# Performance work log

Measured on AMD Instinct MI355X. Metric: run time of the kernel, lower is better.

## Reference

```python
import jax, jax.numpy as jnp
import numpy as np

D = 1152      # model dim
E = 4         # num_experts
HID = 768     # llama FFN hidden: multiple_of*ceil(int(2*1152/3)/256)
NH = 8        # cross-attention heads
TEMP = 2.0    # expert gumbel temperature (eval: no decay)


def _gumbel_softmax(key, logits, temp, hard):
    g = jax.random.gumbel(key, logits.shape, logits.dtype)
    y = jax.nn.softmax((logits + g) / temp, axis=-1)
    if hard:
        oh = jax.nn.one_hot(jnp.argmax(y, axis=-1), logits.shape[-1], dtype=logits.dtype)
        y = oh - jax.lax.stop_gradient(y) + y
    return y


def _mha(x, mem, in_w, in_b, out_w, out_b):
    # torch nn.MultiheadAttention(batch_first=True): packed qkv in_proj.
    B, S, Dm = x.shape
    hd = Dm // NH
    q = x @ in_w[:Dm].T + in_b[:Dm]
    k = mem @ in_w[Dm:2 * Dm].T + in_b[Dm:2 * Dm]
    v = mem @ in_w[2 * Dm:].T + in_b[2 * Dm:]
    q = q.reshape(B, S, NH, hd).transpose(0, 2, 1, 3)
    k = k.reshape(B, -1, NH, hd).transpose(0, 2, 1, 3)
    v = v.reshape(B, -1, NH, hd).transpose(0, 2, 1, 3)
    a = jax.nn.softmax(jnp.einsum('bhqd,bhkd->bhqk', q, k) / jnp.sqrt(jnp.asarray(hd, x.dtype)), axis=-1)
    o = jnp.einsum('bhqk,bhkd->bhqd', a, v).transpose(0, 2, 1, 3).reshape(B, S, Dm)
    return o @ out_w.T + out_b


def _ff_all(x2d, w1, w2, w3):
    # all E llama SwiGLU experts densely: x2d [N,D], w1/w3 [E,HID,D], w2 [E,D,HID] -> [N,E,D]
    h1 = jnp.einsum('nd,ehd->neh', x2d, w1)
    h3 = jnp.einsum('nd,ehd->neh', x2d, w3)
    return jnp.einsum('neh,edh->ned', jax.nn.silu(h1) * h3, w2)


def setup_inputs() -> dict:
    key = jax.random.key(0)
    ks = jax.random.split(key, 32)
    s = 0.02
    B, S, Sc = 2, 1024, 128
    inp = {
        'x': jax.random.normal(ks[0], (B, S, D), jnp.float32),
        'time': jax.random.normal(ks[1], (B, D), jnp.float32),
        'caption': jax.random.normal(ks[2], (B, Sc, D), jnp.float32),
        'acoustic': jax.random.normal(ks[3], (B, S, D), jnp.float32),
        'attn_in_w': jax.random.normal(ks[4], (3 * D, D), jnp.float32) * s,
        'attn_in_b': jnp.zeros((3 * D,), jnp.float32),
        'attn_out_w': jax.random.normal(ks[5], (D, D), jnp.float32) * s,
        'attn_out_b': jnp.zeros((D,), jnp.float32),
        'hl_w': jax.random.normal(ks[6], (2, D), jnp.float32) * s,
        'hl_b': jnp.zeros((2,), jnp.float32),
        'cap_gate_w': jax.random.normal(ks[7], (E, D), jnp.float32) * s,
        'cap_gate_b': jnp.zeros((E,), jnp.float32),
        'ac_gate_w': jax.random.normal(ks[8], (E, D), jnp.float32) * s,
        'ac_gate_b': jnp.zeros((E,), jnp.float32),
        'cap_w1': jax.random.normal(ks[9], (E, HID, D), jnp.float32) * s,
        'cap_w2': jax.random.normal(ks[10], (E, D, HID), jnp.float32) * s,
        'cap_w3': jax.random.normal(ks[11], (E, HID, D), jnp.float32) * s,
        'ac_w1': jax.random.normal(ks[12], (E, HID, D), jnp.float32) * s,
        'ac_w2': jax.random.normal(ks[13], (E, D, HID), jnp.float32) * s,
        'ac_w3': jax.random.normal(ks[14], (E, HID, D), jnp.float32) * s,
        'fr_w1': jax.random.normal(ks[15], (E, HID, D), jnp.float32) * s,
        'fr_w2': jax.random.normal(ks[16], (E, D, HID), jnp.float32) * s,
        'fr_w3': jax.random.normal(ks[17], (E, HID, D), jnp.float32) * s,
    }
    return inp


def reference(x, time, caption, acoustic,
              attn_in_w, attn_in_b, attn_out_w, attn_out_b,
              hl_w, hl_b, cap_gate_w, cap_gate_b, ac_gate_w, ac_gate_b,
              cap_w1, cap_w2, cap_w3, ac_w1, ac_w2, ac_w3,
              fr_w1, fr_w2, fr_w3):
    B, S, Dm = x.shape
    # cross-attention: x attends over caption, output replaces caption stream
    ca = _mha(x, caption, attn_in_w, attn_in_b, attn_out_w, attn_out_b)
    cap2 = ca.reshape(-1, Dm)          # [N, D]
    x2 = x.reshape(-1, Dm)             # [N, D]
    ac2 = acoustic.reshape(-1, Dm)     # [N, D]
    # high-level caption/acoustic gate from time embedding, broadcast over tokens
    hl = jnp.repeat(time @ hl_w.T + hl_b, S, axis=0)  # [N, 2]
    k1, k2, k3 = jax.random.split(jax.random.key(42), 3)
    hp = _gumbel_softmax(k1, hl, 1.0, False)
    cm = hp[:, 0:1]   # caption mask [N,1]
    am = hp[:, 1:2]   # acoustic mask [N,1]
    # expert gates (eval: hard one-hot straight-through)
    cp = _gumbel_softmax(k2, cap2 @ cap_gate_w.T + cap_gate_b, TEMP, True)  # [N,E]
    ap = _gumbel_softmax(k3, ac2 @ ac_gate_w.T + ac_gate_b, TEMP, True)    # [N,E]
    # dense per-expert SwiGLU, masked combine
    zc = jnp.einsum('ned,ne->nd', _ff_all(x2, cap_w1, cap_w2, cap_w3), cp) * cm
    za = jnp.einsum('ned,ne->nd', _ff_all(x2, ac_w1, ac_w2, ac_w3), ap) * am
    y = (zc + za).reshape(B, S, Dm)
    # frequency experts: each expert sees y masked to its channel block, keeps its block
    r = Dm // E
    region = ((jnp.arange(Dm)[None, :] // r) == jnp.arange(E)[:, None]).astype(x.dtype)  # [E,D]
    ym = y[None] * region[:, None, None, :]  # [E,B,S,D]
    h1 = jnp.einsum('ebsd,ehd->ebsh', ym, fr_w1)
    h3 = jnp.einsum('ebsd,ehd->ebsh', ym, fr_w3)
    fo = jnp.einsum('ebsh,edh->ebsd', jax.nn.silu(h1) * h3, fr_w2)  # [E,B,S,D]
    z = jnp.concatenate([fo[e, :, :, e * r:(e + 1) * r] for e in range(E)], axis=-1)
    # load balancing loss
    probs = jnp.concatenate([cp, ap], axis=1)                                  # [N,2E]
    masks = jnp.concatenate([jnp.tile(cm, (1, E)), jnp.tile(am, (1, E))], axis=1)
    usage = (probs * masks).sum(axis=0) / (masks.sum() + 1e-10)
    lb_loss = jnp.mean(usage * jnp.log(usage + 1e-10))
    return z, lb_loss
```

## Files before the change

kernel.cpp:

```cpp
#include <hip/hip_runtime.h>
#include <stdint.h>

#define NDIM 1152
#define NEXP 4
#define NHID 768
#define NHEAD 8
#define HDIM 144
#define NB 2
#define NS 1024
#define NSC 128
#define NTOK 2048
#define NCAP 256

typedef _Float16 f16;
typedef _Float16 f16x4 __attribute__((ext_vector_type(4)));
typedef _Float16 f16x8 __attribute__((ext_vector_type(8)));
typedef float f32x4 __attribute__((ext_vector_type(4)));

#define MFMA16(a, b, c) __builtin_amdgcn_mfma_f32_16x16x32_f16(a, b, c, 0, 0, 0)

#define WSZ ((size_t)NEXP * NHID * NDIM)

__device__ inline uint2 tfry(uint32_t k0, uint32_t k1, uint32_t x0, uint32_t x1) {
  uint32_t k2 = k0 ^ k1 ^ 0x1BD11BDAu;
#define RND(r) { x0 += x1; x1 = (x1 << r) | (x1 >> (32 - r)); x1 ^= x0; }
  x0 += k0; x1 += k1;
  RND(13) RND(15) RND(26) RND(6)
  x0 += k1; x1 += k2 + 1u;
  RND(17) RND(29) RND(16) RND(24)
  x0 += k2; x1 += k0 + 2u;
  RND(13) RND(15) RND(26) RND(6)
  x0 += k0; x1 += k1 + 3u;
  RND(17) RND(29) RND(16) RND(24)
  x0 += k1; x1 += k2 + 4u;
  RND(13) RND(15) RND(26) RND(6)
  x0 += k2; x1 += k0 + 5u;
#undef RND
  return make_uint2(x0, x1);
}

__device__ inline float b2g(uint32_t bits) {
  uint32_t fb = (bits >> 9) | 0x3f800000u;
  float f = __uint_as_float(fb) - 1.0f;
  const float tiny = 1.1754943508222875e-38f;
  float u = f * 1.0f + tiny;
  u = fmaxf(tiny, u);
  return -logf(-logf(u));
}

__global__ void k_prep(const float* __restrict__ timep, const float* __restrict__ hlw,
                       const float* __restrict__ hlb,
                       float* __restrict__ g1, float* __restrict__ g2, float* __restrict__ g3,
                       float* __restrict__ tl) {
  int t = threadIdx.x;
  uint2 k1 = tfry(0u, 42u, 0u, 0u);
  uint2 k2 = tfry(0u, 42u, 0u, 1u);
  uint2 k3 = tfry(0u, 42u, 0u, 2u);
  for (int p = t; p < 4096; p += 256) {
    uint2 o = tfry(k1.x, k1.y, 0u, (uint32_t)p);
    g1[p] = b2g(o.x ^ o.y);
  }
  for (int p = t; p < 8192; p += 256) {
    uint2 o2 = tfry(k2.x, k2.y, 0u, (uint32_t)p);
    g2[p] = b2g(o2.x ^ o2.y);
    uint2 o3 = tfry(k3.x, k3.y, 0u, (uint32_t)p);
    g3[p] = b2g(o3.x ^ o3.y);
  }
  int wv = t >> 6, lane = t & 63;
  {
    int b = wv >> 1, j = wv & 1;
    float s = 0.f;
    for (int k = lane; k < NDIM; k += 64) s += timep[b * NDIM + k] * hlw[j * NDIM + k];
    for (int m = 32; m; m >>= 1) s += __shfl_xor(s, m);
    if (lane == 0) tl[b * 2 + j] = s + hlb[j];
  }
}

__global__ void k_ac_logits(const float* __restrict__ ac, const float* __restrict__ agw,
                            const float* __restrict__ agb, float* __restrict__ al) {
  int wv = threadIdx.x >> 6, lane = threadIdx.x & 63;
  int n = blockIdx.x * 4 + wv;
  float s[NEXP] = {0.f, 0.f, 0.f, 0.f};
  for (int d = lane; d < NDIM; d += 64) {
    float a = ac[(size_t)n * NDIM + d];
#pragma unroll
    for (int e = 0; e < NEXP; ++e) s[e] += a * agw[e * NDIM + d];
  }
#pragma unroll
  for (int e = 0; e < NEXP; ++e)
    for (int m = 32; m; m >>= 1) s[e] += __shfl_xor(s[e], m);
  if (lane == 0) {
#pragma unroll
    for (int e = 0; e < NEXP; ++e) al[n * NEXP + e] = s[e] + agb[e];
  }
}

__global__ void k_cvt_w(const float* __restrict__ s0, const float* __restrict__ s1,
                        const float* __restrict__ s2, const float* __restrict__ s3,
                        const float* __restrict__ s4, const float* __restrict__ s5,
                        const float* __restrict__ s6, const float* __restrict__ s7,
                        const float* __restrict__ s8, f16* __restrict__ dst) {
  int slot = blockIdx.y;
  const float* src;
  switch (slot) {
    case 0: src = s0; break; case 1: src = s1; break; case 2: src = s2; break;
    case 3: src = s3; break; case 4: src = s4; break; case 5: src = s5; break;
    case 6: src = s6; break; case 7: src = s7; break; default: src = s8; break;
  }
  size_t i = ((size_t)blockIdx.x * 256 + threadIdx.x) * 4;
  if (i + 3 < WSZ) {
    float4 v = *(const float4*)(src + i);
    f16x4 h; h[0] = (f16)v.x; h[1] = (f16)v.y; h[2] = (f16)v.z; h[3] = (f16)v.w;
    *(f16x4*)(dst + slot * WSZ + i) = h;
  }
}

__global__ void k_cvt_add(const float* __restrict__ srca, const float* __restrict__ srcb,
                          f16* __restrict__ dst, int n) {
  int i = (blockIdx.x * 256 + threadIdx.x) * 4;
  if (i + 3 < n) {
    float4 va = *(const float4*)(srca + i);
    float4 vb = *(const float4*)(srcb + i);
    f16x4 h;
    h[0] = (f16)(va.x + vb.x); h[1] = (f16)(va.y + vb.y);
    h[2] = (f16)(va.z + vb.z); h[3] = (f16)(va.w + vb.w);
    *(f16x4*)(dst + i) = h;
  }
}

__global__ void k_cvt_split(const float* __restrict__ src, f16* __restrict__ hi,
                            f16* __restrict__ lo, int n) {
  int i = (blockIdx.x * 256 + threadIdx.x) * 4;
  if (i + 3 < n) {
    float4 v = *(const float4*)(src + i);
    f16x4 h, l;
    h[0] = (f16)v.x; l[0] = (f16)((v.x - (float)h[0]) * 2048.f);
    h[1] = (f16)v.y; l[1] = (f16)((v.y - (float)h[1]) * 2048.f);
    h[2] = (f16)v.z; l[2] = (f16)((v.z - (float)h[2]) * 2048.f);
    h[3] = (f16)v.w; l[3] = (f16)((v.w - (float)h[3]) * 2048.f);
    *(f16x4*)(hi + i) = h;
    *(f16x4*)(lo + i) = l;
  }
}

__global__ __launch_bounds__(256) void k_gemm_qkv(
    const f16* __restrict__ xhi, const f16* __restrict__ xlo,
    const f16* __restrict__ caphi, const f16* __restrict__ caplo,
    const float* __restrict__ inw, const float* __restrict__ inb,
    f16* __restrict__ qhi, f16* __restrict__ qlo,
    f16* __restrict__ khi, f16* __restrict__ klo,
    f16* __restrict__ vthi, f16* __restrict__ vtlo) {
  int z = blockIdx.z;
  int M = (z == 0) ? NTOK : NCAP;
  int mt = blockIdx.y, nt = blockIdx.x;
  if (mt * 64 >= M) return;
  const f16* Ah_g = (z == 0) ? xhi : caphi;
  const f16* Al_g = (z == 0) ? xlo : caplo;
  __shared__ f16 Ash[64 * 72];
  __shared__ f16 Asl[64 * 72];
  __shared__ f16 Bsh[64 * 72];
  __shared__ f16 Bsl[64 * 72];
  int t = threadIdx.x;
  int wv = t >> 6, lane = t & 63, m16 = lane & 15, quad = lane >> 4;
  int r0 = t >> 3, ak = (t & 7) * 8;
  size_t a0o = (size_t)(mt * 64 + r0) * NDIM;
  size_t a1o = (size_t)(mt * 64 + r0 + 32) * NDIM;
  f32x4 zf = {0.f, 0.f, 0.f, 0.f};
  f32x4 ah[2][2] = {{zf, zf}, {zf, zf}};
  f32x4 am[2][2] = {{zf, zf}, {zf, zf}};
  uint4 rah0, rah1, ral0, ral1;
  float4 rbw[4];
  rah0 = *(const uint4*)(Ah_g + a0o + ak);
  rah1 = *(const uint4*)(Ah_g + a1o + ak);
  ral0 = *(const uint4*)(Al_g + a0o + ak);
  ral1 = *(const uint4*)(Al_g + a1o + ak);
#pragma unroll
  for (int uu = 0; uu < 4; ++uu) {
    int u = t + uu * 256;
    int rr = u >> 4, kp = (u & 15) * 4;
    rbw[uu] = *(const float4*)(inw + (size_t)(z * NDIM + nt * 64 + rr) * NDIM + kp);
  }
  for (int kc = 0; kc < NDIM; kc += 64) {
    __syncthreads();
    *(uint4*)&Ash[r0 * 72 + ak] = rah0;
    *(uint4*)&Ash[(r0 + 32) * 72 + ak] = rah1;
    *(uint4*)&Asl[r0 * 72 + ak] = ral0;
    *(uint4*)&Asl[(r0 + 32) * 72 + ak] = ral1;
#pragma unroll
    for (int uu = 0; uu < 4; ++uu) {
      int u = t + uu * 256;
      int rr = u >> 4, kp = (u & 15) * 4;
      f16x4 hb, lb;
      hb[0] = (f16)rbw[uu].x; lb[0] = (f16)((rbw[uu].x - (float)hb[0]) * 2048.f);
      hb[1] = (f16)rbw[uu].y; lb[1] = (f16)((rbw[uu].y - (float)hb[1]) * 2048.f);
      hb[2] = (f16)rbw[uu].z; lb[2] = (f16)((rbw[uu].z - (float)hb[2]) * 2048.f);
      hb[3] = (f16)rbw[uu].w; lb[3] = (f16)((rbw[uu].w - (float)hb[3]) * 2048.f);
      *(f16x4*)&Bsh[rr * 72 + kp] = hb;
      *(f16x4*)&Bsl[rr * 72 + kp] = lb;
    }
    __syncthreads();
    int kn = kc + 64;
    if (kn < NDIM) {
      rah0 = *(const uint4*)(Ah_g + a0o + kn + ak);
      rah1 = *(const uint4*)(Ah_g + a1o + kn + ak);
      ral0 = *(const uint4*)(Al_g + a0o + kn + ak);
      ral1 = *(const uint4*)(Al_g + a1o + kn + ak);
#pragma unroll
      for (int uu = 0; uu < 4; ++uu) {
        int u = t + uu * 256;
        int rr = u >> 4, kp = (u & 15) * 4;
        rbw[uu] = *(const float4*)(inw + (size_t)(z * NDIM + nt * 64 + rr) * NDIM + kn + kp);
      }
    }
#pragma unroll
    for (int ks = 0; ks < 2; ++ks) {
      int aoff = ((wv & 1) * 32 + m16) * 72 + ks * 32 + quad * 8;
      int boff = ((wv >> 1) * 32 + m16) * 72 + ks * 32 + quad * 8;
      f16x8 a0h = *(const f16x8*)&Ash[aoff];
      f16x8 a1h = *(const f16x8*)&Ash[aoff + 16 * 72];
      f16x8 a0l = *(const f16x8*)&Asl[aoff];
      f16x8 a1l = *(const f16x8*)&Asl[aoff + 16 * 72];
      f16x8 b0h = *(const f16x8*)&Bsh[boff];
      f16x8 b1h = *(const f16x8*)&Bsh[boff + 16 * 72];
      f16x8 b0l = *(const f16x8*)&Bsl[boff];
      f16x8 b1l = *(const f16x8*)&Bsl[boff + 16 * 72];
      ah[0][0] = MFMA16(a0h, b0h, ah[0][0]);
      ah[0][1] = MFMA16(a0h, b1h, ah[0][1]);
      ah[1][0] = MFMA16(a1h, b0h, ah[1][0]);
      ah[1][1] = MFMA16(a1h, b1h, ah[1][1]);
      am[0][0] = MFMA16(a0h, b0l, am[0][0]);
      am[0][1] = MFMA16(a0h, b1l, am[0][1]);
      am[1][0] = MFMA16(a1h, b0l, am[1][0]);
      am[1][1] = MFMA16(a1h, b1l, am[1][1]);
      am[0][0] = MFMA16(a0l, b0h, am[0][0]);
      am[0][1] = MFMA16(a0l, b1h, am[0][1]);
      am[1][0] = MFMA16(a1l, b0h, am[1][0]);
      am[1][1] = MFMA16(a1l, b1h, am[1][1]);
    }
  }
#pragma unroll
  for (int mi = 0; mi < 2; ++mi)
#pragma unroll
    for (int ni = 0; ni < 2; ++ni)
#pragma unroll
      for (int r = 0; r < 4; ++r) {
        int row = mt * 64 + (wv & 1) * 32 + mi * 16 + quad * 4 + r;
        int col = nt * 64 + (wv >> 1) * 32 + ni * 16 + m16;
        float v = ah[mi][ni][r] + am[mi][ni][r] * (1.f / 2048.f) + inb[z * NDIM + col];
        size_t idx = (size_t)row * NDIM + col;
        if (z == 0) {
          f16 hq = (f16)v;
          qhi[idx] = hq;
          qlo[idx] = (f16)((v - (float)hq) * 2048.f);
        } else if (z == 1) {
          f16 hk = (f16)v;
          khi[idx] = hk;
          klo[idx] = (f16)((v - (float)hk) * 2048.f);
        } else {
          f16 hv = (f16)v;
          int bb = row >> 7, kv = row & 127;
          size_t ti = (size_t)(bb * NDIM + col) * NSC + kv;
          vthi[ti] = hv;
          vtlo[ti] = (f16)((v - (float)hv) * 2048.f);
        }
      }
}

__global__ __launch_bounds__(256) void k_attn(
    const f16* __restrict__ qhi, const f16* __restrict__ qlo,
    const f16* __restrict__ khi, const f16* __restrict__ klo,
    const f16* __restrict__ vthi, const f16* __restrict__ vtlo,
    f16* __restrict__ ohi, f16* __restrict__ olo) {
  int mt = blockIdx.x, bh = blockIdx.y;
  int b = bh >> 3, h = bh & 7;
  __shared__ f16 Ah[64 * 160];
  __shared__ f16 Al[64 * 160];
  __shared__ f16 Bh[32 * 160];
  __shared__ f16 Bl[32 * 160];
  __shared__ f16 Ph[64 * 136];
  __shared__ f16 Pl[64 * 136];
  int t = threadIdx.x;
  int wv = t >> 6, lane = t & 63, m16 = lane & 15, quad = lane >> 4;
  for (int u = t; u < 64 * 20; u += 256) {
    int r = u / 20, kp = (u % 20) * 8;
    uint4 vh = make_uint4(0u, 0u, 0u, 0u), vl = vh;
    if (kp < HDIM) {
      size_t gi = (size_t)(b * NS + mt * 64 + r) * NDIM + h * HDIM + kp;
      vh = *(const uint4*)&qhi[gi];
      vl = *(const uint4*)&qlo[gi];
    }
    *(uint4*)&Ah[r * 160 + kp] = vh;
    *(uint4*)&Al[r * 160 + kp] = vl;
  }
  __syncthreads();
  f16x8 ahf[5], alf[5];
#pragma unroll
  for (int ks = 0; ks < 5; ++ks) {
    int ao = (wv * 16 + m16) * 160 + ks * 32 + quad * 8;
    ahf[ks] = *(const f16x8*)&Ah[ao];
    alf[ks] = *(const f16x8*)&Al[ao];
  }
  f32x4 zf = {0.f, 0.f, 0.f, 0.f};
  f32x4 sh_[4][2], sm_[4][2];
#pragma unroll
  for (int kt = 0; kt < 4; ++kt)
#pragma unroll
    for (int ni = 0; ni < 2; ++ni) { sh_[kt][ni] = zf; sm_[kt][ni] = zf; }
  for (int kt = 0; kt < 4; ++kt) {
    if (kt) __syncthreads();
    for (int u = t; u < 32 * 20; u += 256) {
      int r = u / 20, kp = (u % 20) * 8;
      uint4 vh = make_uint4(0u, 0u, 0u, 0u), vl = vh;
      if (kp < HDIM) {
        size_t gi = (size_t)(b * NSC + kt * 32 + r) * NDIM + h * HDIM + kp;
        vh = *(const uint4*)&khi[gi];
        vl = *(const uint4*)&klo[gi];
      }
      *(uint4*)&Bh[r * 160 + kp] = vh;
      *(uint4*)&Bl[r * 160 + kp] = vl;
    }
    __syncthreads();
#pragma unroll
    for (int ks = 0; ks < 5; ++ks) {
#pragma unroll
      for (int ni = 0; ni < 2; ++ni) {
        int bo = (ni * 16 + m16) * 160 + ks * 32 + quad * 8;
        f16x8 bhf = *(const f16x8*)&Bh[bo];
        f16x8 blf = *(const f16x8*)&Bl[bo];
        sh_[kt][ni] = MFMA16(ahf[ks], bhf, sh_[kt][ni]);
        sm_[kt][ni] = MFMA16(ahf[ks], blf, sm_[kt][ni]);
        sm_[kt][ni] = MFMA16(alf[ks], bhf, sm_[kt][ni]);
      }
    }
  }
  float sv[4][2][4];
  float mx[4] = {-1e30f, -1e30f, -1e30f, -1e30f};
#pragma unroll
  for (int kt = 0; kt < 4; ++kt)
#pragma unroll
    for (int ni = 0; ni < 2; ++ni)
#pragma unroll
      for (int r = 0; r < 4; ++r) {
        float s = (sh_[kt][ni][r] + sm_[kt][ni][r] * (1.f / 2048.f)) * (1.f / 12.f);
        sv[kt][ni][r] = s;
        mx[r] = fmaxf(mx[r], s);
      }
#pragma unroll
  for (int r = 0; r < 4; ++r) {
    mx[r] = fmaxf(mx[r], __shfl_xor(mx[r], 1));
    mx[r] = fmaxf(mx[r], __shfl_xor(mx[r], 2));
    mx[r] = fmaxf(mx[r], __shfl_xor(mx[r], 4));
    mx[r] = fmaxf(mx[r], __shfl_xor(mx[r], 8));
  }
  float sum[4] = {0.f, 0.f, 0.f, 0.f};
#pragma unroll
  for (int kt = 0; kt < 4; ++kt)
#pragma unroll
    for (int ni = 0; ni < 2; ++ni)
#pragma unroll
      for (int r = 0; r < 4; ++r) {
        float e = expf(sv[kt][ni][r] - mx[r]);
        sv[kt][ni][r] = e;
        sum[r] += e;
      }
  float inv[4];
#pragma unroll
  for (int r = 0; r < 4; ++r) {
    sum[r] += __shfl_xor(sum[r], 1);
    sum[r] += __shfl_xor(sum[r], 2);
    sum[r] += __shfl_xor(sum[r], 4);
    sum[r] += __shfl_xor(sum[r], 8);
    inv[r] = 1.0f / sum[r];
  }
#pragma unroll
  for (int kt = 0; kt < 4; ++kt)
#pragma unroll
    for (int ni = 0; ni < 2; ++ni)
#pragma unroll
      for (int r = 0; r < 4; ++r) {
        float p = sv[kt][ni][r] * inv[r];
        int row = wv * 16 + quad * 4 + r;
        int col = kt * 32 + ni * 16 + m16;
        f16 ph = (f16)p;
        Ph[row * 136 + col] = ph;
        Pl[row * 136 + col] = (f16)((p - (float)ph) * 2048.f);
      }
  const f16* vbh = vthi + (size_t)(b * NDIM + h * HDIM) * NSC;
  const f16* vbl = vtlo + (size_t)(b * NDIM + h * HDIM) * NSC;
  f32x4 oh_[9], om_[9];
#pragma unroll
  for (int nb = 0; nb < 9; ++nb) { oh_[nb] = zf; om_[nb] = zf; }
#pragma unroll
  for (int ks = 0; ks < 4; ++ks) {
    int po = (wv * 16 + m16) * 136 + ks * 32 + quad * 8;
    f16x8 pah = *(const f16x8*)&Ph[po];
    f16x8 pal = *(const f16x8*)&Pl[po];
#pragma unroll
    for (int nb = 0; nb < 9; ++nb) {
      size_t vo = (size_t)(nb * 16 + m16) * NSC + ks * 32 + quad * 8;
      f16x8 bvh = *(const f16x8*)&vbh[vo];
      f16x8 bvl = *(const f16x8*)&vbl[vo];
      oh_[nb] = MFMA16(pah, bvh, oh_[nb]);
      om_[nb] = MFMA16(pah, bvl, om_[nb]);
      om_[nb] = MFMA16(pal, bvh, om_[nb]);
    }
  }
#pragma unroll
  for (int nb = 0; nb < 9; ++nb)
#pragma unroll
    for (int r = 0; r < 4; ++r) {
      int row = mt * 64 + wv * 16 + quad * 4 + r;
      int col = h * HDIM + nb * 16 + m16;
      float v = oh_[nb][r] + om_[nb][r] * (1.f / 2048.f);
      size_t idx = (size_t)(b * NS + row) * NDIM + col;
      f16 hv = (f16)v;
      ohi[idx] = hv;
      olo[idx] = (f16)((v - (float)hv) * 2048.f);
    }
}

__global__ __launch_bounds__(256) void k_ca(
    const f16* __restrict__ ohi, const f16* __restrict__ olo,
    const float* __restrict__ ow, const float* __restrict__ ob,
    float* __restrict__ ca) {
  int mt = blockIdx.y, nt = blockIdx.x;
  __shared__ f16 Ash[64 * 72];
  __shared__ f16 Asl[64 * 72];
  __shared__ f16 Bsh[64 * 72];
  __shared__ f16 Bsl[64 * 72];
  int t = threadIdx.x;
  int wv = t >> 6, lane = t & 63, m16 = lane & 15, quad = lane >> 4;
  int r0 = t >> 3, ak = (t & 7) * 8;
  size_t a0o = (size_t)(mt * 64 + r0) * NDIM;
  size_t a1o = (size_t)(mt * 64 + r0 + 32) * NDIM;
  f32x4 zf = {0.f, 0.f, 0.f, 0.f};
  f32x4 ah[2][2] = {{zf, zf}, {zf, zf}};
  f32x4 am[2][2] = {{zf, zf}, {zf, zf}};
  uint4 rah0, rah1, ral0, ral1;
  float4 rbw[4];
  rah0 = *(const uint4*)(ohi + a0o + ak);
  rah1 = *(const uint4*)(ohi + a1o + ak);
  ral0 = *(const uint4*)(olo + a0o + ak);
  ral1 = *(const uint4*)(olo + a1o + ak);
#pragma unroll
  for (int uu = 0; uu < 4; ++uu) {
    int u = t + uu * 256;
    int rr = u >> 4, kp = (u & 15) * 4;
    rbw[uu] = *(const float4*)(ow + (size_t)(nt * 64 + rr) * NDIM + kp);
  }
  for (int kc = 0; kc < NDIM; kc += 64) {
    __syncthreads();
    *(uint4*)&Ash[r0 * 72 + ak] = rah0;
    *(uint4*)&Ash[(r0 + 32) * 72 + ak] = rah1;
    *(uint4*)&Asl[r0 * 72 + ak] = ral0;
    *(uint4*)&Asl[(r0 + 32) * 72 + ak] = ral1;
#pragma unroll
    for (int uu = 0; uu < 4; ++uu) {
      int u = t + uu * 256;
      int rr = u >> 4, kp = (u & 15) * 4;
      f16x4 hb, lb;
      hb[0] = (f16)rbw[uu].x; lb[0] = (f16)((rbw[uu].x - (float)hb[0]) * 2048.f);
      hb[1] = (f16)rbw[uu].y; lb[1] = (f16)((rbw[uu].y - (float)hb[1]) * 2048.f);
      hb[2] = (f16)rbw[uu].z; lb[2] = (f16)((rbw[uu].z - (float)hb[2]) * 2048.f);
      hb[3] = (f16)rbw[uu].w; lb[3] = (f16)((rbw[uu].w - (float)hb[3]) * 2048.f);
      *(f16x4*)&Bsh[rr * 72 + kp] = hb;
      *(f16x4*)&Bsl[rr * 72 + kp] = lb;
    }
    __syncthreads();
    int kn = kc + 64;
    if (kn < NDIM) {
      rah0 = *(const uint4*)(ohi + a0o + kn + ak);
      rah1 = *(const uint4*)(ohi + a1o + kn + ak);
      ral0 = *(const uint4*)(olo + a0o + kn + ak);
      ral1 = *(const uint4*)(olo + a1o + kn + ak);
#pragma unroll
      for (int uu = 0; uu < 4; ++uu) {
        int u = t + uu * 256;
        int rr = u >> 4, kp = (u & 15) * 4;
        rbw[uu] = *(const float4*)(ow + (size_t)(nt * 64 + rr) * NDIM + kn + kp);
      }
    }
#pragma unroll
    for (int ks = 0; ks < 2; ++ks) {
      int aoff = ((wv & 1) * 32 + m16) * 72 + ks * 32 + quad * 8;
      int boff = ((wv >> 1) * 32 + m16) * 72 + ks * 32 + quad * 8;
      f16x8 a0h = *(const f16x8*)&Ash[aoff];
      f16x8 a1h = *(const f16x8*)&Ash[aoff + 16 * 72];
      f16x8 a0l = *(const f16x8*)&Asl[aoff];
      f16x8 a1l = *(const f16x8*)&Asl[aoff + 16 * 72];
      f16x8 b0h = *(const f16x8*)&Bsh[boff];
      f16x8 b1h = *(const f16x8*)&Bsh[boff + 16 * 72];
      f16x8 b0l = *(const f16x8*)&Bsl[boff];
      f16x8 b1l = *(const f16x8*)&Bsl[boff + 16 * 72];
      ah[0][0] = MFMA16(a0h, b0h, ah[0][0]);
      ah[0][1] = MFMA16(a0h, b1h, ah[0][1]);
      ah[1][0] = MFMA16(a1h, b0h, ah[1][0]);
      ah[1][1] = MFMA16(a1h, b1h, ah[1][1]);
      am[0][0] = MFMA16(a0h, b0l, am[0][0]);
      am[0][1] = MFMA16(a0h, b1l, am[0][1]);
      am[1][0] = MFMA16(a1h, b0l, am[1][0]);
      am[1][1] = MFMA16(a1h, b1l, am[1][1]);
      am[0][0] = MFMA16(a0l, b0h, am[0][0]);
      am[0][1] = MFMA16(a0l, b1h, am[0][1]);
      am[1][0] = MFMA16(a1l, b0h, am[1][0]);
      am[1][1] = MFMA16(a1l, b1h, am[1][1]);
    }
  }
#pragma unroll
  for (int mi = 0; mi < 2; ++mi)
#pragma unroll
    for (int ni = 0; ni < 2; ++ni)
#pragma unroll
      for (int r = 0; r < 4; ++r) {
        int row = mt * 64 + (wv & 1) * 32 + mi * 16 + quad * 4 + r;
        int col = nt * 64 + (wv >> 1) * 32 + ni * 16 + m16;
        ca[(size_t)row * NDIM + col] =
            ah[mi][ni][r] + am[mi][ni][r] * (1.f / 2048.f) + ob[col];
      }
}

__global__ __launch_bounds__(1024) void k_route(
    const float* __restrict__ cl, const float* __restrict__ al,
    const float* __restrict__ g1, const float* __restrict__ g2,
    const float* __restrict__ g3, const float* __restrict__ tl,
    float* __restrict__ cmv, float* __restrict__ amv,
    int* __restrict__ lists, int* __restrict__ counts, float* __restrict__ out_loss) {
  __shared__ int lcnt[8];
  __shared__ float bins[8];
  __shared__ float ssum[2];
  int t = threadIdx.x;
  if (t < 8) { lcnt[t] = 0; bins[t] = 0.f; }
  if (t < 2) ssum[t] = 0.f;
  __syncthreads();
  for (int n = t; n < NTOK; n += 1024) {
    float lc[NEXP];
#pragma unroll
    for (int e = 0; e < NEXP; ++e) lc[e] = cl[n * NEXP + e] + g2[n * 4 + e];
    int ec = 0; float bv = lc[0];
#pragma unroll
    for (int e = 1; e < NEXP; ++e) if (lc[e] > bv) { bv = lc[e]; ec = e; }
    float la[NEXP];
#pragma unroll
    for (int e = 0; e < NEXP; ++e) la[e] = al[n * NEXP + e] + g3[n * 4 + e];
    int ea = 0; float bva = la[0];
#pragma unroll
    for (int e = 1; e < NEXP; ++e) if (la[e] > bva) { bva = la[e]; ea = e; }
    int b = n >> 10;
    float a0 = tl[b * 2 + 0] + g1[n * 2 + 0];
    float a1 = tl[b * 2 + 1] + g1[n * 2 + 1];
    float mx = fmaxf(a0, a1);
    float e0 = expf(a0 - mx), e1 = expf(a1 - mx);
    float cm = e0 / (e0 + e1), am = e1 / (e0 + e1);
    cmv[n] = cm; amv[n] = am;
    int p0 = atomicAdd(&lcnt[ec], 1);
    lists[ec * NTOK + p0] = n;
    int p1 = atomicAdd(&lcnt[4 + ea], 1);
    lists[(4 + ea) * NTOK + p1] = n;
    atomicAdd(&bins[ec], cm);
    atomicAdd(&bins[4 + ea], am);
    atomicAdd(&ssum[0], cm);
    atomicAdd(&ssum[1], am);
  }
  __syncthreads();
  if (t < 8) counts[t] = lcnt[t];
  if (t == 0) {
    float denom = 4.f * (ssum[0] + ssum[1]) + 1e-10f;
    float acc = 0.f;
    for (int j = 0; j < 8; ++j) {
      float u = bins[j] / denom;
      acc += u * logf(u + 1e-10f);
    }
    out_loss[0] = acc / 8.f;
  }
}

__global__ __launch_bounds__(256) void k_gemm1(
    const f16* __restrict__ x16, const f16* __restrict__ y16,
    const f16* __restrict__ wf,
    const int* __restrict__ lists, const int* __restrict__ counts,
    f16* __restrict__ tbuf, int gbase, int G) {
  int bid = blockIdx.x;
  int xcd = bid & 7;
  int local = bid >> 3;
  int ppx = (G * 12) >> 3;
  int pair = xcd * ppx + (local >> 5);
  int mt = local & 31;
  int g = gbase + pair / 12;
  int nt = pair % 12;
  const f16* A; const f16* B1; const f16* B3; f16* tout;
  const int* list = nullptr;
  int cnt, koff, K;
  if (g < 8) {
    int e = g & 3;
    cnt = counts[g];
    list = lists + g * NTOK;
    A = x16; koff = 0; K = NDIM;
    B1 = wf + (size_t)((g < 4) ? 0 : 2) * WSZ + (size_t)e * NHID * NDIM;
    B3 = wf + (size_t)((g < 4) ? 1 : 3) * WSZ + (size_t)e * NHID * NDIM;
    tout = tbuf + (size_t)g * NTOK * NHID;
  } else {
    int e = g - 8;
    cnt = NTOK;
    A = y16; koff = e * 288; K = 288;
    B1 = wf + (size_t)4 * WSZ + (size_t)e * NHID * NDIM + koff;
    B3 = wf + (size_t)5 * WSZ + (size_t)e * NHID * NDIM + koff;
    tout = tbuf + (size_t)e * NTOK * NHID;
  }
  if (mt * 64 >= cnt) return;
  int t = threadIdx.x;
  int wv = t >> 6, lane = t & 63, m16 = lane & 15, quad = lane >> 4;
  int r0 = t >> 3, ak = (t & 7) * 8;
  int m0 = mt * 64 + r0, m1 = m0 + 32;
  int tok0, tok1;
  if (list) { tok0 = list[min(m0, cnt - 1)]; tok1 = list[min(m1, cnt - 1)]; }
  else { tok0 = m0; tok1 = m1; }
  const f16* ar0 = A + (size_t)tok0 * NDIM + koff;
  const f16* ar1 = A + (size_t)tok1 * NDIM + koff;
  const f16* b1r0 = B1 + (size_t)(nt * 64 + r0) * NDIM;
  const f16* b1r1 = B1 + (size_t)(nt * 64 + r0 + 32) * NDIM;
  const f16* b3r0 = B3 + (size_t)(nt * 64 + r0) * NDIM;
  const f16* b3r1 = B3 + (size_t)(nt * 64 + r0 + 32) * NDIM;
  __shared__ f16 As[64 * 72];
  __shared__ f16 Bs1[64 * 72];
  __shared__ f16 Bs2[64 * 72];
  f32x4 zf = {0.f, 0.f, 0.f, 0.f};
  f32x4 ac1[2][2] = {{zf, zf}, {zf, zf}};
  f32x4 ac2[2][2] = {{zf, zf}, {zf, zf}};
  uint4 z4u = make_uint4(0u, 0u, 0u, 0u);
  uint4 ra0, ra1, rb10, rb11, rb30, rb31;
  {
    bool v = (ak < K);
    ra0  = v ? *(const uint4*)(ar0 + ak) : z4u;
    ra1  = v ? *(const uint4*)(ar1 + ak) : z4u;
    rb10 = v ? *(const uint4*)(b1r0 + ak) : z4u;
    rb11 = v ? *(const uint4*)(b1r1 + ak) : z4u;
    rb30 = v ? *(const uint4*)(b3r0 + ak) : z4u;
    rb31 = v ? *(const uint4*)(b3r1 + ak) : z4u;
  }
  for (int kc = 0; kc < K; kc += 64) {
    __syncthreads();
    *(uint4*)&As[r0 * 72 + ak] = ra0;
    *(uint4*)&As[(r0 + 32) * 72 + ak] = ra1;
    *(uint4*)&Bs1[r0 * 72 + ak] = rb10;
    *(uint4*)&Bs1[(r0 + 32) * 72 + ak] = rb11;
    *(uint4*)&Bs2[r0 * 72 + ak] = rb30;
    *(uint4*)&Bs2[(r0 + 32) * 72 + ak] = rb31;
    __syncthreads();
    int kn = kc + 64;
    if (kn < K) {
      bool v = (kn + ak < K);
      ra0  = v ? *(const uint4*)(ar0 + kn + ak) : z4u;
      ra1  = v ? *(const uint4*)(ar1 + kn + ak) : z4u;
      rb10 = v ? *(const uint4*)(b1r0 + kn + ak) : z4u;
      rb11 = v ? *(const uint4*)(b1r1 + kn + ak) : z4u;
      rb30 = v ? *(const uint4*)(b3r0 + kn + ak) : z4u;
      rb31 = v ? *(const uint4*)(b3r1 + kn + ak) : z4u;
    }
#pragma unroll
    for (int ks = 0; ks < 2; ++ks) {
      int aoff = ((wv & 1) * 32 + m16) * 72 + ks * 32 + quad * 8;
      int boff = ((wv >> 1) * 32 + m16) * 72 + ks * 32 + quad * 8;
      f16x8 a0 = *(const f16x8*)&As[aoff];
      f16x8 a1 = *(const f16x8*)&As[aoff + 16 * 72];
      f16x8 b10 = *(const f16x8*)&Bs1[boff];
      f16x8 b11 = *(const f16x8*)&Bs1[boff + 16 * 72];
      f16x8 b30 = *(const f16x8*)&Bs2[boff];
      f16x8 b31 = *(const f16x8*)&Bs2[boff + 16 * 72];
      ac1[0][0] = MFMA16(a0, b10, ac1[0][0]);
      ac1[0][1] = MFMA16(a0, b11, ac1[0][1]);
      ac1[1][0] = MFMA16(a1, b10, ac1[1][0]);
      ac1[1][1] = MFMA16(a1, b11, ac1[1][1]);
      ac2[0][0] = MFMA16(a0, b30, ac2[0][0]);
      ac2[0][1] = MFMA16(a0, b31, ac2[0][1]);
      ac2[1][0] = MFMA16(a1, b30, ac2[1][0]);
      ac2[1][1] = MFMA16(a1, b31, ac2[1][1]);
    }
  }
#pragma unroll
  for (int mi = 0; mi < 2; ++mi)
#pragma unroll
    for (int ni = 0; ni < 2; ++ni)
#pragma unroll
      for (int r = 0; r < 4; ++r) {
        int row = mt * 64 + (wv & 1) * 32 + mi * 16 + quad * 4 + r;
        int col = nt * 64 + (wv >> 1) * 32 + ni * 16 + m16;
        float h1 = ac1[mi][ni][r];
        float h3 = ac2[mi][ni][r];
        float sl = h1 / (1.0f + expf(-h1));
        tout[(size_t)row * NHID + col] = (f16)(sl * h3);
      }
}

__global__ __launch_bounds__(256) void k_gemm2(
    const f16* __restrict__ tbuf, const f16* __restrict__ wf,
    const int* __restrict__ lists, const int* __restrict__ counts,
    const float* __restrict__ cmv, const float* __restrict__ amv,
    float* __restrict__ yc, float* __restrict__ ya) {
  int bid = blockIdx.x;
  int xcd = bid & 7;
  int local = bid >> 3;
  int pair = xcd * 18 + (local >> 5);
  int mt = local & 31;
  int g = pair / 18;
  int nt = pair % 18;
  int e = g & 3;
  int cnt = counts[g];
  if (mt * 64 >= cnt) return;
  const int* list = lists + g * NTOK;
  const f16* A = tbuf + (size_t)g * NTOK * NHID;
  const f16* Bw = wf + (size_t)((g < 4) ? 6 : 7) * WSZ + (size_t)e * NDIM * NHID;
  const float* sc = (g < 4) ? cmv : amv;
  float* y = (g < 4) ? yc : ya;
  int t = threadIdx.x;
  int wv = t >> 6, lane = t & 63, m16 = lane & 15, quad = lane >> 4;
  int r0 = t >> 3, ak = (t & 7) * 8;
  const f16* ar0 = A + (size_t)(mt * 64 + r0) * NHID;
  const f16* ar1 = A + (size_t)(mt * 64 + r0 + 32) * NHID;
  const f16* br0 = Bw + (size_t)(nt * 64 + r0) * NHID;
  const f16* br1 = Bw + (size_t)(nt * 64 + r0 + 32) * NHID;
  __shared__ f16 As[64 * 72];
  __shared__ f16 Bs[64 * 72];
  f32x4 zf = {0.f, 0.f, 0.f, 0.f};
  f32x4 acc[2][2] = {{zf, zf}, {zf, zf}};
  uint4 ra0, ra1, rb0, rb1;
  ra0 = *(const uint4*)(ar0 + ak);
  ra1 = *(const uint4*)(ar1 + ak);
  rb0 = *(const uint4*)(br0 + ak);
  rb1 = *(const uint4*)(br1 + ak);
  for (int kc = 0; kc < NHID; kc += 64) {
    __syncthreads();
    *(uint4*)&As[r0 * 72 + ak] = ra0;
    *(uint4*)&As[(r0 + 32) * 72 + ak] = ra1;
    *(uint4*)&Bs[r0 * 72 + ak] = rb0;
    *(uint4*)&Bs[(r0 + 32) * 72 + ak] = rb1;
    __syncthreads();
    int kn = kc + 64;
    if (kn < NHID) {
      ra0 = *(const uint4*)(ar0 + kn + ak);
      ra1 = *(const uint4*)(ar1 + kn + ak);
      rb0 = *(const uint4*)(br0 + kn + ak);
      rb1 = *(const uint4*)(br1 + kn + ak);
    }
#pragma unroll
    for (int ks = 0; ks < 2; ++ks) {
      int aoff = ((wv & 1) * 32 + m16) * 72 + ks * 32 + quad * 8;
      int boff = ((wv >> 1) * 32 + m16) * 72 + ks * 32 + quad * 8;
      f16x8 a0 = *(const f16x8*)&As[aoff];
      f16x8 a1 = *(const f16x8*)&As[aoff + 16 * 72];
      f16x8 b0 = *(const f16x8*)&Bs[boff];
      f16x8 b1 = *(const f16x8*)&Bs[boff + 16 * 72];
      acc[0][0] = MFMA16(a0, b0, acc[0][0]);
      acc[0][1] = MFMA16(a0, b1, acc[0][1]);
      acc[1][0] = MFMA16(a1, b0, acc[1][0]);
      acc[1][1] = MFMA16(a1, b1, acc[1][1]);
    }
  }
#pragma unroll
  for (int mi = 0; mi < 2; ++mi)
#pragma unroll
    for (int ni = 0; ni < 2; ++ni)
#pragma unroll
      for (int r = 0; r < 4; ++r) {
        int mg = mt * 64 + (wv & 1) * 32 + mi * 16 + quad * 4 + r;
        if (mg < cnt) {
          int tok = list[mg];
          int col = nt * 64 + (wv >> 1) * 32 + ni * 16 + m16;
          float v = acc[mi][ni][r] * sc[tok];
          y[(size_t)tok * NDIM + col] = v;
        }
      }
}

__global__ __launch_bounds__(256) void k_gemm2_fr(
    const f16* __restrict__ tbuf, const f16* __restrict__ wf, float* __restrict__ zz) {
  int e = blockIdx.z;
  int mt = blockIdx.y, nt = blockIdx.x;
  const f16* A = tbuf + (size_t)e * NTOK * NHID;
  const f16* Bw = wf + (size_t)8 * WSZ + (size_t)e * NDIM * NHID;
  int t = threadIdx.x;
  int wv = t >> 6, lane = t & 63, m16 = lane & 15, quad = lane >> 4;
  int r0 = t >> 3, ak = (t & 7) * 8;
  const f16* ar0 = A + (size_t)(mt * 64 + r0) * NHID;
  const f16* ar1 = A + (size_t)(mt * 64 + r0 + 32) * NHID;
  int ne0 = min(nt * 64 + r0, 287), ne1 = min(nt * 64 + r0 + 32, 287);
  const f16* br0 = Bw + (size_t)(e * 288 + ne0) * NHID;
  const f16* br1 = Bw + (size_t)(e * 288 + ne1) * NHID;
  __shared__ f16 As[64 * 72];
  __shared__ f16 Bs[64 * 72];
  f32x4 zf = {0.f, 0.f, 0.f, 0.f};
  f32x4 acc[2][2] = {{zf, zf}, {zf, zf}};
  uint4 ra0, ra1, rb0, rb1;
  ra0 = *(const uint4*)(ar0 + ak);
  ra1 = *(const uint4*)(ar1 + ak);
  rb0 = *(const uint4*)(br0 + ak);
  rb1 = *(const uint4*)(br1 + ak);
  for (int kc = 0; kc < NHID; kc += 64) {
    __syncthreads();
    *(uint4*)&As[r0 * 72 + ak] = ra0;
    *(uint4*)&As[(r0 + 32) * 72 + ak] = ra1;
    *(uint4*)&Bs[r0 * 72 + ak] = rb0;
    *(uint4*)&Bs[(r0 + 32) * 72 + ak] = rb1;
    __syncthreads();
    int kn = kc + 64;
    if (kn < NHID) {
      ra0 = *(const uint4*)(ar0 + kn + ak);
      ra1 = *(const uint4*)(ar1 + kn + ak);
      rb0 = *(const uint4*)(br0 + kn + ak);
      rb1 = *(const uint4*)(br1 + kn + ak);
    }
#pragma unroll
    for (int ks = 0; ks < 2; ++ks) {
      int aoff = ((wv & 1) * 32 + m16) * 72 + ks * 32 + quad * 8;
      int boff = ((wv >> 1) * 32 + m16) * 72 + ks * 32 + quad * 8;
      f16x8 a0 = *(const f16x8*)&As[aoff];
      f16x8 a1 = *(const f16x8*)&As[aoff + 16 * 72];
      f16x8 b0 = *(const f16x8*)&Bs[boff];
      f16x8 b1 = *(const f16x8*)&Bs[boff + 16 * 72];
      acc[0][0] = MFMA16(a0, b0, acc[0][0]);
      acc[0][1] = MFMA16(a0, b1, acc[0][1]);
      acc[1][0] = MFMA16(a1, b0, acc[1][0]);
      acc[1][1] = MFMA16(a1, b1, acc[1][1]);
    }
  }
#pragma unroll
  for (int mi = 0; mi < 2; ++mi)
#pragma unroll
    for (int ni = 0; ni < 2; ++ni)
#pragma unroll
      for (int r = 0; r < 4; ++r) {
        int cg = nt * 64 + (wv >> 1) * 32 + ni * 16 + m16;
        if (cg < 288) {
          int row = mt * 64 + (wv & 1) * 32 + mi * 16 + quad * 4 + r;
          zz[(size_t)row * NDIM + e * 288 + cg] = acc[mi][ni][r];
        }
      }
}

extern "C" void kernel_launch(void* const* d_in, const int* in_sizes, int n_in,
                              void* d_out, int out_size, void* d_ws, size_t ws_size,
                              hipStream_t stream) {
  const float* x          = (const float*)d_in[0];
  const float* timep      = (const float*)d_in[1];
  const float* caption    = (const float*)d_in[2];
  const float* acoustic   = (const float*)d_in[3];
  const float* attn_in_w  = (const float*)d_in[4];
  const float* attn_in_b  = (const float*)d_in[5];
  const float* attn_out_w = (const float*)d_in[6];
  const float* attn_out_b = (const float*)d_in[7];
  const float* hl_w       = (const float*)d_in[8];
  const float* hl_b       = (const float*)d_in[9];
  const float* cap_gate_w = (const float*)d_in[10];
  const float* cap_gate_b = (const float*)d_in[11];
  const float* ac_gate_w  = (const float*)d_in[12];
  const float* ac_gate_b  = (const float*)d_in[13];
  const float* cap_w1     = (const float*)d_in[14];
  const float* cap_w2     = (const float*)d_in[15];
  const float* cap_w3     = (const float*)d_in[16];
  const float* ac_w1      = (const float*)d_in[17];
  const float* ac_w2      = (const float*)d_in[18];
  const float* ac_w3      = (const float*)d_in[19];
  const float* fr_w1      = (const float*)d_in[20];
  const float* fr_w2      = (const float*)d_in[21];
  const float* fr_w3      = (const float*)d_in[22];
  (void)in_sizes; (void)n_in; (void)out_size; (void)ws_size;

  float* zout = (float*)d_out;
  float* loss = zout + (size_t)NTOK * NDIM;

  char* wsb = (char*)d_ws;
  size_t off = 0;
  auto alloc = [&](size_t bytes) -> void* {
    void* p = wsb + off;
    off = (off + bytes + 255) & ~(size_t)255;
    return p;
  };
  float* g1     = (float*)alloc(4096 * 4);
  float* g2     = (float*)alloc(8192 * 4);
  float* g3     = (float*)alloc(8192 * 4);
  float* tl     = (float*)alloc(4 * 4);
  float* al     = (float*)alloc((size_t)NTOK * NEXP * 4);
  float* cl     = (float*)alloc((size_t)NTOK * NEXP * 4);
  float* cmv    = (float*)alloc((size_t)NTOK * 4);
  float* amv    = (float*)alloc((size_t)NTOK * 4);
  int*   lists  = (int*)alloc((size_t)8 * NTOK * 4);
  int*   counts = (int*)alloc(8 * 4);
  f16*   xhi    = (f16*)alloc((size_t)NTOK * NDIM * 2);
  f16*   wf16   = (f16*)alloc((size_t)9 * WSZ * 2);
  size_t region = off;
  f16*   xlo    = (f16*)alloc((size_t)NTOK * NDIM * 2);
  f16*   caphi  = (f16*)alloc((size_t)NCAP * NDIM * 2);
  f16*   caplo  = (f16*)alloc((size_t)NCAP * NDIM * 2);
  f16*   qhi    = (f16*)alloc((size_t)NTOK * NDIM * 2);
  f16*   qlo    = (f16*)alloc((size_t)NTOK * NDIM * 2);
  f16*   khi    = (f16*)alloc((size_t)NCAP * NDIM * 2);
  f16*   klo    = (f16*)alloc((size_t)NCAP * NDIM * 2);
  f16*   vthi   = (f16*)alloc((size_t)NB * NDIM * NSC * 2);
  f16*   vtlo   = (f16*)alloc((size_t)NB * NDIM * NSC * 2);
  f16*   ohi    = (f16*)alloc((size_t)NTOK * NDIM * 2);
  f16*   olo    = (f16*)alloc((size_t)NTOK * NDIM * 2);
  float* ca32   = (float*)alloc((size_t)NTOK * NDIM * 4);
  off = region;
  f16*   tbuf   = (f16*)alloc((size_t)8 * NTOK * NHID * 2);
  float* ybc    = (float*)alloc((size_t)NTOK * NDIM * 4);
  float* yba    = (float*)alloc((size_t)NTOK * NDIM * 4);
  f16*   y16    = (f16*)alloc((size_t)NTOK * NDIM * 2);

  k_prep<<<dim3(1), dim3(256), 0, stream>>>(timep, hl_w, hl_b, g1, g2, g3, tl);
  k_ac_logits<<<dim3(512), dim3(256), 0, stream>>>(acoustic, ac_gate_w, ac_gate_b, al);
  k_cvt_split<<<dim3(2304), dim3(256), 0, stream>>>(x, xhi, xlo, NTOK * NDIM);
  k_cvt_split<<<dim3(288), dim3(256), 0, stream>>>(caption, caphi, caplo, NCAP * NDIM);
  k_gemm_qkv<<<dim3(18, 32, 3), dim3(256), 0, stream>>>(xhi, xlo, caphi, caplo,
                                                        attn_in_w, attn_in_b,
                                                        qhi, qlo, khi, klo, vthi, vtlo);
  k_attn<<<dim3(16, 16), dim3(256), 0, stream>>>(qhi, qlo, khi, klo, vthi, vtlo, ohi, olo);
  k_ca<<<dim3(18, 32), dim3(256), 0, stream>>>(ohi, olo, attn_out_w, attn_out_b, ca32);
  k_ac_logits<<<dim3(512), dim3(256), 0, stream>>>(ca32, cap_gate_w, cap_gate_b, cl);
  k_route<<<dim3(1), dim3(1024), 0, stream>>>(cl, al, g1, g2, g3, tl,
                                              cmv, amv, lists, counts, loss);
  k_cvt_w<<<dim3(3456, 9), dim3(256), 0, stream>>>(cap_w1, cap_w3, ac_w1, ac_w3,
                                                   fr_w1, fr_w3, cap_w2, ac_w2, fr_w2,
                                                   wf16);
  k_gemm1<<<dim3(3072), dim3(256), 0, stream>>>(xhi, y16, wf16, lists, counts, tbuf, 0, 8);
  k_gemm2<<<dim3(4608), dim3(256), 0, stream>>>(tbuf, wf16, lists, counts,
                                                cmv, amv, ybc, yba);
  k_cvt_add<<<dim3(2304), dim3(256), 0, stream>>>(ybc, yba, y16, NTOK * NDIM);
  k_gemm1<<<dim3(1536), dim3(256), 0, stream>>>(xhi, y16, wf16, lists, counts, tbuf, 8, 4);
  k_gemm2_fr<<<dim3(5, 32, 4), dim3(256), 0, stream>>>(tbuf, wf16, zout);
}
```

Before: 491.4 us.

## Fold expert weight fp16 conversion into QKV GEMM launch as extra z-slices

Removes the standalone weight-conversion kernel and runs the conversion as extra grid z-slices of the QKV projection kernel. Each block converts 2048 floats (8 per thread) instead of 1024, so fewer blocks are needed. The bandwidth-bound conversion can overlap with the compute-bound QKV GEMM and one launch is saved. In exchange the two kinds of work compete for memory bandwidth and CUs within one launch.

After: 476.4 us. -3.0%, faster.

```diff
diff --git a/kernel.cpp b/kernel.cpp
--- a/kernel.cpp
+++ b/kernel.cpp
@@ -20,6 +20,8 @@
 #define MFMA16(a, b, c) __builtin_amdgcn_mfma_f32_16x16x32_f16(a, b, c, 0, 0, 0)
 
 #define WSZ ((size_t)NEXP * NHID * NDIM)
+#define CVT_BLOCKS 15552
+#define CVT_ZS 27
 
 __device__ inline uint2 tfry(uint32_t k0, uint32_t k1, uint32_t x0, uint32_t x1) {
   uint32_t k2 = k0 ^ k1 ^ 0x1BD11BDAu;
@@ -95,26 +97,6 @@
   }
 }
 
-__global__ void k_cvt_w(const float* __restrict__ s0, const float* __restrict__ s1,
-                        const float* __restrict__ s2, const float* __restrict__ s3,
-                        const float* __restrict__ s4, const float* __restrict__ s5,
-                        const float* __restrict__ s6, const float* __restrict__ s7,
-                        const float* __restrict__ s8, f16* __restrict__ dst) {
-  int slot = blockIdx.y;
-  const float* src;
-  switch (slot) {
-    case 0: src = s0; break; case 1: src = s1; break; case 2: src = s2; break;
-    case 3: src = s3; break; case 4: src = s4; break; case 5: src = s5; break;
-    case 6: src = s6; break; case 7: src = s7; break; default: src = s8; break;
-  }
-  size_t i = ((size_t)blockIdx.x * 256 + threadIdx.x) * 4;
-  if (i + 3 < WSZ) {
-    float4 v = *(const float4*)(src + i);
-    f16x4 h; h[0] = (f16)v.x; h[1] = (f16)v.y; h[2] = (f16)v.z; h[3] = (f16)v.w;
-    *(f16x4*)(dst + slot * WSZ + i) = h;
-  }
-}
-
 __global__ void k_cvt_add(const float* __restrict__ srca, const float* __restrict__ srcb,
                           f16* __restrict__ dst, int n) {
   int i = (blockIdx.x * 256 + threadIdx.x) * 4;
@@ -149,8 +131,31 @@
     const float* __restrict__ inw, const float* __restrict__ inb,
     f16* __restrict__ qhi, f16* __restrict__ qlo,
     f16* __restrict__ khi, f16* __restrict__ klo,
-    f16* __restrict__ vthi, f16* __restrict__ vtlo) {
+    f16* __restrict__ vthi, f16* __restrict__ vtlo,
+    const float* __restrict__ w0, const float* __restrict__ w1,
+    const float* __restrict__ w2, const float* __restrict__ w3,
+    const float* __restrict__ w4, const float* __restrict__ w5,
+    const float* __restrict__ w6, const float* __restrict__ w7,
+    const float* __restrict__ w8, f16* __restrict__ wf16) {
   int z = blockIdx.z;
+  if (z >= 3) {
+    int gid = (z - 3) * 576 + blockIdx.y * 18 + blockIdx.x;
+    int slot = gid / 1728;
+    const float* src;
+    switch (slot) {
+      case 0: src = w0; break; case 1: src = w1; break; case 2: src = w2; break;
+      case 3: src = w3; break; case 4: src = w4; break; case 5: src = w5; break;
+      case 6: src = w6; break; case 7: src = w7; break; default: src = w8; break;
+    }
+    size_t off = (size_t)(gid % 1728) * 2048 + (size_t)threadIdx.x * 8;
+    float4 v0 = *(const float4*)(src + off);
+    float4 v1 = *(const float4*)(src + off + 4);
+    f16x8 h;
+    h[0] = (f16)v0.x; h[1] = (f16)v0.y; h[2] = (f16)v0.z; h[3] = (f16)v0.w;
+    h[4] = (f16)v1.x; h[5] = (f16)v1.y; h[6] = (f16)v1.z; h[7] = (f16)v1.w;
+    *(f16x8*)(wf16 + (size_t)slot * WSZ + off) = h;
+    return;
+  }
   int M = (z == 0) ? NTOK : NCAP;
   int mt = blockIdx.y, nt = blockIdx.x;
   if (mt * 64 >= M) return;
@@ -909,17 +914,15 @@
   k_ac_logits<<<dim3(512), dim3(256), 0, stream>>>(acoustic, ac_gate_w, ac_gate_b, al);
   k_cvt_split<<<dim3(2304), dim3(256), 0, stream>>>(x, xhi, xlo, NTOK * NDIM);
   k_cvt_split<<<dim3(288), dim3(256), 0, stream>>>(caption, caphi, caplo, NCAP * NDIM);
-  k_gemm_qkv<<<dim3(18, 32, 3), dim3(256), 0, stream>>>(xhi, xlo, caphi, caplo,
-                                                        attn_in_w, attn_in_b,
-                                                        qhi, qlo, khi, klo, vthi, vtlo);
+  k_gemm_qkv<<<dim3(18, 32, 3 + CVT_ZS), dim3(256), 0, stream>>>(
+      xhi, xlo, caphi, caplo, attn_in_w, attn_in_b,
+      qhi, qlo, khi, klo, vthi, vtlo,
+      cap_w1, cap_w3, ac_w1, ac_w3, fr_w1, fr_w3, cap_w2, ac_w2, fr_w2, wf16);
   k_attn<<<dim3(16, 16), dim3(256), 0, stream>>>(qhi, qlo, khi, klo, vthi, vtlo, ohi, olo);
   k_ca<<<dim3(18, 32), dim3(256), 0, stream>>>(ohi, olo, attn_out_w, attn_out_b, ca32);
   k_ac_logits<<<dim3(512), dim3(256), 0, stream>>>(ca32, cap_gate_w, cap_gate_b, cl);
   k_route<<<dim3(1), dim3(1024), 0, stream>>>(cl, al, g1, g2, g3, tl,
                                               cmv, amv, lists, counts, loss);
-  k_cvt_w<<<dim3(3456, 9), dim3(256), 0, stream>>>(cap_w1, cap_w3, ac_w1, ac_w3,
-                                                   fr_w1, fr_w3, cap_w2, ac_w2, fr_w2,
-                                                   wf16);
   k_gemm1<<<dim3(3072), dim3(256), 0, stream>>>(xhi, y16, wf16, lists, counts, tbuf, 0, 8);
   k_gemm2<<<dim3(4608), dim3(256), 0, stream>>>(tbuf, wf16, lists, counts,
                                                 cmv, amv, ybc, yba);
```
